# Kernel optimization log

Hardware: AMD Instinct MI355X
Metric: run time of the kernel (lower is better)

The kernel has to match this reference:

```python
import jax, jax.numpy as jnp
import numpy as np

VERY_NEG = -1e11
VERY_SMALL = 1e-10
PAGERANK_LAMBDA = 0.8
FACT_SCALE = 3.0


def _linear(x, W, b):
    return x @ W.T + b


def _lstm(x, Wih, Whh, bih, bhh):
    # single-layer unidirectional LSTM, pytorch gate order (i, f, g, o)
    B, T, _ = x.shape
    H = Whh.shape[1]
    def step(carry, xt):
        h, c = carry
        g = xt @ Wih.T + bih + h @ Whh.T + bhh
        i, f, gg, o = jnp.split(g, 4, axis=-1)
        c = jax.nn.sigmoid(f) * c + jax.nn.sigmoid(i) * jnp.tanh(gg)
        h = jax.nn.sigmoid(o) * jnp.tanh(c)
        return (h, c), h
    init = (jnp.zeros((B, H), x.dtype), jnp.zeros((B, H), x.dtype))
    (h_last, _), hs = jax.lax.scan(step, init, jnp.swapaxes(x, 0, 1))
    return jnp.swapaxes(hs, 0, 1), h_last


def _forward(local_entity, q2e_adj_mat, kb_fact_rel, query_text, e2f_entity, f2e_entity,
             answer_dist, word_emb, entity_emb, rel_emb, ent_W, ent_b, rel_W, rel_b,
             lstm_Wih, lstm_Whh, lstm_bih, lstm_bhh, q2e_W, q2e_b, head_W, head_b,
             tail_W, tail_b, self_W, self_b, e2e_W, e2e_b, score_W, score_b):
    B, E = local_entity.shape
    D = ent_W.shape[0]
    num_word = word_emb.shape[0] - 1
    num_entity = entity_emb.shape[0] - 1
    b_idx = jnp.arange(B)[:, None]  # (B,1) for batched gather/scatter

    # --- query LSTM encoder ---
    query_mask = (query_text != num_word).astype(jnp.float32)            # (B,Q)
    qh, q_last = _lstm(word_emb[query_text], lstm_Wih, lstm_Whh, lstm_bih, lstm_bhh)
    query_node_emb = q_last[:, None, :]                                   # (B,1,D)

    # --- fact embeddings + fact-query attention weights ---
    local_fact_emb = _linear(rel_emb[kb_fact_rel], rel_W, rel_b)          # (B,F,D)
    div = jnp.sqrt(jnp.asarray(D, jnp.float32))
    sim = jnp.einsum('bqd,bfd->bqf', qh, local_fact_emb) / div
    sim = jax.nn.softmax(sim + (1.0 - query_mask)[:, :, None] * VERY_NEG, axis=1)
    att = jnp.einsum('bqf,bqd->bfd', sim, qh)                             # (B,F,D)
    Wf = jnp.sum(att * local_fact_emb, axis=2) / div                      # (B,F)
    W_tilde = jnp.exp(Wf - jnp.max(Wf, axis=1, keepdims=True))
    # e2f_softmax[b,e] = sum of W_tilde over facts whose head is e (sparse e2f^T @ W_tilde)
    e2f_softmax = jnp.maximum(
        jnp.zeros((B, E), jnp.float32).at[b_idx, e2f_entity].add(W_tilde), VERY_SMALL)

    # --- entity embeddings (word_dim != entity_dim -> entity_linear) ---
    local_entity_emb = _linear(entity_emb[local_entity], ent_W, ent_b)    # (B,E,D)
    pagerank_f = q2e_adj_mat[:, :, 0]                                     # (B,E)

    n_layer = q2e_W.shape[0]
    for i in range(n_layer):
        q2e_emb = jnp.broadcast_to(_linear(query_node_emb, q2e_W[i], q2e_b[i]), (B, E, D))
        # entity -> fact: gather head-entity messages
        head = _linear(local_entity_emb, head_W[i], head_b[i])            # (B,E,D)
        e2f_emb = jax.nn.relu(
            _linear(local_fact_emb, self_W[i], self_b[i]) + head[b_idx, e2f_entity])
        pr = pagerank_f / e2f_softmax                                     # (B,E)
        e2f_norm = (W_tilde * pr[b_idx, e2f_entity])[:, :, None]          # (B,F,1)
        e2f_emb = e2f_emb * e2f_norm
        # fact -> entity: scatter-add to tail entities
        tail = _linear(e2f_emb, tail_W[i], tail_b[i])                     # (B,F,D)
        f2e_emb = jax.nn.relu(
            _linear(local_entity_emb, self_W[i], self_b[i])
            + jnp.zeros((B, E, D), jnp.float32).at[b_idx, f2e_entity].add(tail))
        pagerank_f = (PAGERANK_LAMBDA
                      * jnp.zeros((B, E), jnp.float32).at[b_idx, f2e_entity].add(e2f_norm[:, :, 0])
                      + (1.0 - PAGERANK_LAMBDA) * pagerank_f)
        nxt = jnp.concatenate([local_entity_emb, q2e_emb, FACT_SCALE * f2e_emb], axis=2)
        local_entity_emb = jax.nn.relu(_linear(nxt, e2e_W[i], e2e_b[i]))

    score = local_entity_emb @ score_W + score_b                          # (B,E)
    mask = (local_entity != num_entity).astype(jnp.float32)
    score = score + (1.0 - mask) * VERY_NEG
    return jax.nn.sigmoid(score) * mask


def setup_inputs() -> dict:
    key = jax.random.key(0)
    ks = jax.random.split(key, 24)
    B, E, Fc, Q = 8, 2000, 12000, 20
    WD, D = 300, 100
    NE, NW, NR, L = 100000, 40000, 300, 3
    f32 = jnp.float32
    def nrm(k, shape, scale):
        return jax.random.normal(k, shape, f32) * scale
    return {
        'local_entity': jax.random.randint(ks[0], (B, E), 0, NE),
        'q2e_adj_mat': jax.random.uniform(ks[1], (B, E, 1), f32),
        'kb_fact_rel': jax.random.randint(ks[2], (B, Fc), 0, NR),
        'query_text': jax.random.randint(ks[3], (B, Q), 0, NW),
        'e2f_entity': jax.random.randint(ks[4], (B, Fc), 0, E),
        'f2e_entity': jax.random.randint(ks[5], (B, Fc), 0, E),
        'answer_dist': jax.random.uniform(ks[6], (B, E), f32),
        'word_emb': nrm(ks[7], (NW + 1, WD), 0.02),
        'entity_emb': nrm(ks[8], (NE + 1, WD), 0.02),
        'rel_emb': nrm(ks[9], (NR + 1, 2 * WD), 0.02),
        'ent_W': nrm(ks[10], (D, WD), WD ** -0.5), 'ent_b': jnp.zeros((D,), f32),
        'rel_W': nrm(ks[11], (D, 2 * WD), (2 * WD) ** -0.5), 'rel_b': jnp.zeros((D,), f32),
        'lstm_Wih': nrm(ks[12], (4 * D, WD), WD ** -0.5),
        'lstm_Whh': nrm(ks[13], (4 * D, D), D ** -0.5),
        'lstm_bih': jnp.zeros((4 * D,), f32), 'lstm_bhh': jnp.zeros((4 * D,), f32),
        'q2e_W': nrm(ks[14], (L, D, D), D ** -0.5), 'q2e_b': jnp.zeros((L, D), f32),
        'head_W': nrm(ks[15], (L, D, D), D ** -0.5), 'head_b': jnp.zeros((L, D), f32),
        'tail_W': nrm(ks[16], (L, D, D), D ** -0.5), 'tail_b': jnp.zeros((L, D), f32),
        'self_W': nrm(ks[17], (L, D, D), D ** -0.5), 'self_b': jnp.zeros((L, D), f32),
        'e2e_W': nrm(ks[18], (L, D, 3 * D), (3 * D) ** -0.5), 'e2e_b': jnp.zeros((L, D), f32),
        'score_W': nrm(ks[19], (D,), D ** -0.5), 'score_b': jnp.zeros((), f32),
    }


def reference(local_entity, q2e_adj_mat, kb_fact_rel, query_text, e2f_entity, f2e_entity,
              answer_dist, word_emb, entity_emb, rel_emb, ent_W, ent_b, rel_W, rel_b,
              lstm_Wih, lstm_Whh, lstm_bih, lstm_bhh, q2e_W, q2e_b, head_W, head_b,
              tail_W, tail_b, self_W, self_b, e2e_W, e2e_b, score_W, score_b):
    return _forward(local_entity, q2e_adj_mat, kb_fact_rel, query_text, e2f_entity,
                    f2e_entity, answer_dist, word_emb, entity_emb, rel_emb, ent_W, ent_b,
                    rel_W, rel_b, lstm_Wih, lstm_Whh, lstm_bih, lstm_bhh, q2e_W, q2e_b,
                    head_W, head_b, tail_W, tail_b, self_W, self_b, e2e_W, e2e_b,
                    score_W, score_b)
```

## Files before the change

### kernel.cpp

```cpp
#include <hip/hip_runtime.h>
#include <math.h>

#define VERY_NEG  -100000000000.0f
#define VERY_SMALLF 1e-10f

constexpr int B  = 8;
constexpr int E  = 2000;
constexpr int FC = 12000;
constexpr int Q  = 20;
constexpr int WD = 300;
constexpr int D  = 100;
constexpr int NW = 40000;
constexpr int NE = 100000;
constexpr int G4 = 4 * D;
constexpr int NREL = 301;
constexpr int NF = B * FC;
constexpr int NR_ = B * E;
constexpr int NRP = 16384;

__device__ __forceinline__ float sigmoidf_(float x) { return 1.0f / (1.0f + expf(-x)); }

__device__ __forceinline__ void tile16(const float* __restrict__ As_, const float* __restrict__ Bs_,
                                       int rg, int cgc, float acc[4][4]) {
#pragma unroll 5
    for (int k4 = 0; k4 < 25; ++k4) {
        float a_[4][4], b_[4][4];
#pragma unroll
        for (int i = 0; i < 4; ++i) {
            float4 v = *(const float4*)&As_[(rg * 4 + i) * 104 + k4 * 4];
            a_[i][0] = v.x; a_[i][1] = v.y; a_[i][2] = v.z; a_[i][3] = v.w;
        }
#pragma unroll
        for (int kk = 0; kk < 4; ++kk) {
            float4 v = *(const float4*)&Bs_[(k4 * 4 + kk) * 100 + cgc * 4];
            b_[kk][0] = v.x; b_[kk][1] = v.y; b_[kk][2] = v.z; b_[kk][3] = v.w;
        }
#pragma unroll
        for (int kk = 0; kk < 4; ++kk)
#pragma unroll
            for (int i = 0; i < 4; ++i)
#pragma unroll
                for (int j = 0; j < 4; ++j)
                    acc[i][j] += a_[i][kk] * b_[kk][j];
    }
}

__device__ __forceinline__ void tile8(const float* __restrict__ As_, const float* __restrict__ Bs_,
                                      int rg, int cgc, float acc[2][4]) {
#pragma unroll 5
    for (int k4 = 0; k4 < 25; ++k4) {
        float a_[2][4], b_[4][4];
#pragma unroll
        for (int i = 0; i < 2; ++i) {
            float4 v = *(const float4*)&As_[(rg * 2 + i) * 104 + k4 * 4];
            a_[i][0] = v.x; a_[i][1] = v.y; a_[i][2] = v.z; a_[i][3] = v.w;
        }
#pragma unroll
        for (int kk = 0; kk < 4; ++kk) {
            float4 v = *(const float4*)&Bs_[(k4 * 4 + kk) * 100 + cgc * 4];
            b_[kk][0] = v.x; b_[kk][1] = v.y; b_[kk][2] = v.z; b_[kk][3] = v.w;
        }
#pragma unroll
        for (int kk = 0; kk < 4; ++kk)
#pragma unroll
            for (int i = 0; i < 2; ++i)
#pragma unroll
                for (int j = 0; j < 4; ++j)
                    acc[i][j] += a_[i][kk] * b_[kk][j];
    }
}

__device__ __forceinline__ void stage_B100(const float* __restrict__ Wt, int ldW, int col0, int k0,
                                           float* __restrict__ Bs_) {
    for (int i = threadIdx.x; i < 2500; i += 256) {
        int k = i / 25, d2 = i - k * 25;
        *(float4*)&Bs_[k * 100 + d2 * 4] = *(const float4*)&Wt[(size_t)(k0 + k) * ldW + col0 + d2 * 4];
    }
}

__device__ void gemm_tile_g(const float* __restrict__ A, int K,
                            const int* __restrict__ rix, int nrows,
                            const float* __restrict__ Wt, int ldW, int col0,
                            const float* __restrict__ bias,
                            float* __restrict__ C,
                            int base, float* As_, float* Bs_) {
    int tid = threadIdx.x;
    int cg_ = tid & 31, rg = tid >> 5, cgc = cg_ < 25 ? cg_ : 24;
    float acc[4][4] = {{0.f}};
    for (int k0 = 0; k0 < K; k0 += 100) {
        __syncthreads();
        for (int i = tid; i < 800; i += 256) {
            int r = i / 25, c = i - r * 25;
            int rr = base + r; if (rr >= nrows) rr = nrows - 1;
            int gr = rix ? rix[rr] : rr;
            *(float4*)&As_[r * 104 + c * 4] = *(const float4*)&A[(size_t)gr * K + k0 + c * 4];
        }
        stage_B100(Wt, ldW, col0, k0, Bs_);
        __syncthreads();
        tile16(As_, Bs_, rg, cgc, acc);
    }
    if (cg_ < 25) {
        float4 bb = *(const float4*)&bias[col0 + cg_ * 4];
#pragma unroll
        for (int i = 0; i < 4; ++i) {
            int r = base + rg * 4 + i;
            if (r < nrows) {
                float4 o;
                o.x = acc[i][0] + bb.x; o.y = acc[i][1] + bb.y;
                o.z = acc[i][2] + bb.z; o.w = acc[i][3] + bb.w;
                *(float4*)&C[(size_t)r * ldW + col0 + cg_ * 4] = o;
            }
        }
    }
}

__device__ void gemm_tile_512(const float* __restrict__ A, int K,
                              const int* __restrict__ rix, int nrows,
                              const float* __restrict__ Wt, int ldW, int col0,
                              const float* __restrict__ bias,
                              float* __restrict__ C,
                              int base, float* As_, float* Bs_) {
    int tid = threadIdx.x;
    int cg_ = tid & 31, rg = (tid >> 5) & 7, cgc = cg_ < 25 ? cg_ : 24;
    bool on = tid < 256;
    float acc[4][4] = {{0.f}};
    for (int k0 = 0; k0 < K; k0 += 100) {
        __syncthreads();
        for (int i = tid; i < 800; i += 512) {
            int r = i / 25, c = i - r * 25;
            int rr = base + r; if (rr >= nrows) rr = nrows - 1;
            int gr = rix ? rix[rr] : rr;
            *(float4*)&As_[r * 104 + c * 4] = *(const float4*)&A[(size_t)gr * K + k0 + c * 4];
        }
        for (int i = tid; i < 2500; i += 512) {
            int k = i / 25, d2 = i - k * 25;
            *(float4*)&Bs_[k * 100 + d2 * 4] = *(const float4*)&Wt[(size_t)(k0 + k) * ldW + col0 + d2 * 4];
        }
        __syncthreads();
        if (on) tile16(As_, Bs_, rg, cgc, acc);
    }
    if (on && cg_ < 25) {
        float4 bb = *(const float4*)&bias[col0 + cg_ * 4];
#pragma unroll
        for (int i = 0; i < 4; ++i) {
            int r = base + rg * 4 + i;
            if (r < nrows) {
                float4 o;
                o.x = acc[i][0] + bb.x; o.y = acc[i][1] + bb.y;
                o.z = acc[i][2] + bb.z; o.w = acc[i][3] + bb.w;
                *(float4*)&C[(size_t)r * ldW + col0 + cg_ * 4] = o;
            }
        }
    }
}

struct P0 {
    const float *ent_W, *rel_W, *Wih, *Whh, *head_W, *self_W, *tail_W, *e2e_W, *bih, *bhh, *q2e_adj;
    float *entWt, *relWt, *WihT, *WhhT, *headWt, *selfWt, *tailWt, *e2eWt, *bihh, *pr, *e2f_sm;
    const int *f2e, *kb_rel; int *cnt, *present;
};

__device__ void tr_tile(const float* __restrict__ in, float* __restrict__ out, int M, int K,
                        int kx, int my, float tb[32][33]) {
    int x = threadIdx.x & 31, y = threadIdx.x >> 5;
    int k0 = kx * 32, m0 = my * 32;
    for (int yy = y; yy < 32; yy += 8) {
        int m = m0 + yy, k = k0 + x;
        if (m < M && k < K) tb[yy][x] = in[(size_t)m * K + k];
    }
    __syncthreads();
    for (int yy = y; yy < 32; yy += 8) {
        int k = k0 + yy, m = m0 + x;
        if (m < M && k < K) out[(size_t)k * M + m] = tb[x][yy];
    }
}

__global__ __launch_bounds__(256) void k_prep0(P0 p) {
    __shared__ float tb[32][33];
    int j = blockIdx.x, tid = threadIdx.x;
    if (j < 40)       { tr_tile(p.ent_W, p.entWt, 100, 300, j % 10, j / 10, tb); }
    else if (j < 116) { j -= 40;  tr_tile(p.rel_W, p.relWt, 100, 600, j % 19, j / 19, tb); }
    else if (j < 246) { j -= 116; tr_tile(p.Wih, p.WihT, 400, 300, j % 10, j / 10, tb); }
    else if (j < 298) { j -= 246; tr_tile(p.Whh, p.WhhT, 400, 100, j % 4, j / 4, tb); }
    else if (j < 346) { j -= 298; int z = j / 16, t = j % 16; tr_tile(p.head_W + z * 10000, p.headWt + z * 10000, 100, 100, t % 4, t / 4, tb); }
    else if (j < 394) { j -= 346; int z = j / 16, t = j % 16; tr_tile(p.self_W + z * 10000, p.selfWt + z * 10000, 100, 100, t % 4, t / 4, tb); }
    else if (j < 442) { j -= 394; int z = j / 16, t = j % 16; tr_tile(p.tail_W + z * 10000, p.tailWt + z * 10000, 100, 100, t % 4, t / 4, tb); }
    else if (j < 562) { j -= 442; int z = j / 40, t = j % 40; tr_tile(p.e2e_W + z * 30000, p.e2eWt + z * 30000, 100, 300, t % 10, t / 10, tb); }
    else if (j < 564) { int idx = (j - 562) * 256 + tid; if (idx < G4) p.bihh[idx] = p.bih[idx] + p.bhh[idx]; }
    else if (j < 580) { int idx = (j - 564) * 256 + tid; if (idx < 4000) ((float4*)p.pr)[idx] = ((const float4*)p.q2e_adj)[idx]; }
    else if (j < 596) { int idx = (j - 580) * 256 + tid; if (idx < 4000) ((float4*)p.e2f_sm)[idx] = make_float4(0.f, 0.f, 0.f, 0.f); }
    else {
        int fid = (j - 596) * 256 + tid;
        int b = fid / FC;
        atomicAdd(&p.cnt[b * E + p.f2e[fid]], 1);
        p.present[b * NREL + p.kb_rel[fid]] = 1;
    }
}

struct F1P {
    const int *cnt; int *off, *cursor; float *cnt_f;
    const float *word_emb; const int *qtext; const float *WihT, *bihh; float *xW;
    const float *rel_emb, *relWt, *rel_b; float *rel_proj;
    const float *entity_emb; const int *local_entity;
    const float *entWt, *ent_b, *headWt0, *head_b0, *selfWt0, *self_b0;
    float *lee, *head, *lee_self;
};

__device__ void scan_block(const int* __restrict__ cnt, int* __restrict__ off,
                           int* __restrict__ cursor, float* __restrict__ cnt_f, int* part) {
    int t = threadIdx.x;
    int s = 0;
    const int4* c4 = (const int4*)(cnt + t * 64);
#pragma unroll 4
    for (int i = 0; i < 16; ++i) { int4 v = c4[i]; s += v.x + v.y + v.z + v.w; }
    part[t] = s;
    __syncthreads();
    for (int d = 1; d < 256; d <<= 1) {
        int add = (t >= d) ? part[t - d] : 0;
        __syncthreads();
        part[t] += add;
        __syncthreads();
    }
    int run = part[t] - s;
    for (int i = 0; i < 64; ++i) {
        int idx = t * 64 + i;
        if (idx < NR_) {
            off[idx] = run; cursor[idx] = run; cnt_f[idx] = (float)cnt[idx];
            run += cnt[idx];
        }
    }
    if (t == 255) off[NR_] = part[255];
}

__device__ void lee_dual_tile16(int base, const F1P& p, float* As_, float* Bs_) {
    int tid = threadIdx.x;
    int cg_ = tid & 31, rg = tid >> 5, cgc = cg_ < 25 ? cg_ : 24;
    float acc[2][4] = {{0.f}};
    for (int k0 = 0; k0 < 300; k0 += 100) {
        __syncthreads();
        for (int i = tid; i < 400; i += 256) {
            int r = i / 25, c = i - r * 25;
            int gr = p.local_entity[base + r];
            *(float4*)&As_[r * 104 + c * 4] = *(const float4*)&p.entity_emb[(size_t)gr * 300 + k0 + c * 4];
        }
        stage_B100(p.entWt, 100, 0, k0, Bs_);
        __syncthreads();
        tile8(As_, Bs_, rg, cgc, acc);
    }
    __syncthreads();
    if (cg_ < 25) {
        float4 bb = *(const float4*)&p.ent_b[cg_ * 4];
#pragma unroll
        for (int i = 0; i < 2; ++i) {
            int r = base + rg * 2 + i;
            float4 o;
            o.x = acc[i][0] + bb.x; o.y = acc[i][1] + bb.y;
            o.z = acc[i][2] + bb.z; o.w = acc[i][3] + bb.w;
            *(float4*)&p.lee[(size_t)r * 100 + cg_ * 4] = o;
            *(float4*)&As_[(rg * 2 + i) * 104 + cg_ * 4] = o;
        }
    }
    stage_B100(p.headWt0, 100, 0, 0, Bs_);
    __syncthreads();
    float acc2[2][4] = {{0.f}};
    tile8(As_, Bs_, rg, cgc, acc2);
    if (cg_ < 25) {
        float4 bb = *(const float4*)&p.head_b0[cg_ * 4];
#pragma unroll
        for (int i = 0; i < 2; ++i) {
            int r = base + rg * 2 + i;
            float4 o;
            o.x = acc2[i][0] + bb.x; o.y = acc2[i][1] + bb.y;
            o.z = acc2[i][2] + bb.z; o.w = acc2[i][3] + bb.w;
            *(float4*)&p.head[(size_t)r * 100 + cg_ * 4] = o;
        }
    }
    __syncthreads();
    stage_B100(p.selfWt0, 100, 0, 0, Bs_);
    __syncthreads();
    float acc3[2][4] = {{0.f}};
    tile8(As_, Bs_, rg, cgc, acc3);
    if (cg_ < 25) {
        float4 bb = *(const float4*)&p.self_b0[cg_ * 4];
#pragma unroll
        for (int i = 0; i < 2; ++i) {
            int r = base + rg * 2 + i;
            float4 o;
            o.x = acc3[i][0] + bb.x; o.y = acc3[i][1] + bb.y;
            o.z = acc3[i][2] + bb.z; o.w = acc3[i][3] + bb.w;
            *(float4*)&p.lee_self[(size_t)r * 100 + cg_ * 4] = o;
        }
    }
}

__global__ __launch_bounds__(256) void k_front1(F1P p) {
    __shared__ float smem[13328];
    int j = blockIdx.x;
    if (j == 0) {
        scan_block(p.cnt, p.off, p.cursor, p.cnt_f, (int*)smem);
    } else if (j <= 20) {
        j -= 1;
        gemm_tile_g(p.word_emb, WD, p.qtext, B * Q, p.WihT, G4, (j / 5) * 100, p.bihh,
                    p.xW, (j % 5) * 32, smem, smem + 3328);
    } else if (j <= 30) {
        j -= 21;
        gemm_tile_g(p.rel_emb, 2 * WD, nullptr, NREL, p.relWt, D, 0, p.rel_b,
                    p.rel_proj, j * 32, smem, smem + 3328);
    } else {
        lee_dual_tile16((j - 31) * 16, p, smem, smem + 1664);
    }
}

struct F2P {
    const float *xW, *WhhT, *q2e_W, *q2e_b; float *q2e_vec;
    const int *qtext, *present;
    const float *rel_proj; float *Wt_rel;
    const float *selfWt, *self_b; float *self_proj;
};

__device__ void lstm_wfall_block(int b, const F2P& p, float* smem) {
    float* h    = smem;
    float* c    = smem + 128;
    float* gate = smem + 256;
    float* qh_s = smem + 704;
    float* msk  = smem + 2704;
    float* red  = smem + 2752;
    int t = threadIdx.x;
    float w[100];
    if (t < G4) {
#pragma unroll
        for (int j = 0; j < 100; ++j) w[j] = p.WhhT[j * G4 + t];
    }
    if (t < D) { h[t] = 0.f; c[t] = 0.f; }
    if (t < Q) msk[t] = (p.qtext[b * Q + t] != NW) ? 1.f : 0.f;
    __syncthreads();
    for (int step = 0; step < Q; ++step) {
        if (t < G4) {
            float a0 = 0.f, a1 = 0.f, a2 = 0.f, a3 = 0.f;
#pragma unroll
            for (int k4 = 0; k4 < 25; ++k4) {
                float4 hv = *(const float4*)&h[k4 * 4];
                a0 += hv.x * w[k4 * 4 + 0];
                a1 += hv.y * w[k4 * 4 + 1];
                a2 += hv.z * w[k4 * 4 + 2];
                a3 += hv.w * w[k4 * 4 + 3];
            }
            gate[t] = p.xW[(b * Q + step) * G4 + t] + ((a0 + a1) + (a2 + a3));
        }
        __syncthreads();
        if (t < D) {
            float ig = sigmoidf_(gate[t]);
            float fg = sigmoidf_(gate[D + t]);
            float gg = tanhf(gate[2 * D + t]);
            float og = sigmoidf_(gate[3 * D + t]);
            float cn = fg * c[t] + ig * gg;
            c[t] = cn;
            float hn = og * tanhf(cn);
            h[t] = hn;
            qh_s[step * D + t] = hn;
        }
        __syncthreads();
    }
    if (t < 3 * D) {
        int l = t / D, d = t - l * D;
        float acc = p.q2e_b[l * D + d];
        const float* W = p.q2e_W + (size_t)(l * D + d) * D;
        for (int k = 0; k < D; ++k) acc += h[k] * W[k];
        p.q2e_vec[(l * B + b) * D + d] = acc;
    }
    float wf = 0.f;
    bool active = t < NREL;
    if (active) {
        const float* lfe = p.rel_proj + t * D;
        float s[Q];
#pragma unroll
        for (int q = 0; q < Q; ++q) s[q] = 0.f;
        for (int k = 0; k < D; ++k) {
            float lv = lfe[k];
#pragma unroll
            for (int q = 0; q < Q; ++q) s[q] += qh_s[q * D + k] * lv;
        }
        float m = -INFINITY;
        float sv[Q];
#pragma unroll
        for (int q = 0; q < Q; ++q) {
            s[q] *= 0.1f;
            sv[q] = s[q] + (1.f - msk[q]) * VERY_NEG;
            m = fmaxf(m, sv[q]);
        }
        float sum = 0.f;
        float ex[Q];
#pragma unroll
        for (int q = 0; q < Q; ++q) { ex[q] = expf(sv[q] - m); sum += ex[q]; }
#pragma unroll
        for (int q = 0; q < Q; ++q) wf += (ex[q] / sum) * s[q];
    }
    red[t] = (active && p.present[b * NREL + t]) ? wf : -INFINITY;
    __syncthreads();
    for (int st = 256; st > 0; st >>= 1) {
        if (t < st) red[t] = fmaxf(red[t], red[t + st]);
        __syncthreads();
    }
    if (active) p.Wt_rel[b * NREL + t] = expf(wf - red[0]);
}

__global__ __launch_bounds__(512) void k_front2(F2P p) {
    __shared__ float smem[13328];
    int j = blockIdx.x;
    if (j < 8) {
        lstm_wfall_block(j, p, smem);
    } else {
        j -= 8;
        int z = j / 10, t = j % 10;
        gemm_tile_512(p.rel_proj, D, nullptr, NREL, p.selfWt + z * 10000, D, 0, p.self_b + z * 100,
                      p.self_proj + (size_t)z * NREL * D, t * 32, smem, smem + 3328);
    }
}

__global__ void k_scef(const int* __restrict__ f2e, const int* __restrict__ e2f,
                       const int* __restrict__ kb_rel, const float* __restrict__ Wt_rel,
                       int* __restrict__ cursor, int* __restrict__ sorted,
                       float* __restrict__ W_tilde, float* __restrict__ e2f_sm) {
    int fid = blockIdx.x * 256 + threadIdx.x;
    int b = fid / FC;
    int pos = atomicAdd(&cursor[b * E + f2e[fid]], 1);
    sorted[pos] = fid;
    float wt = Wt_rel[b * NREL + kb_rel[fid]];
    W_tilde[fid] = wt;
    atomicAdd(&e2f_sm[b * E + e2f[fid]], wt);
}

__global__ void k_gfact(const int* __restrict__ sorted, const int* __restrict__ kb_rel,
                        const int* __restrict__ e2f, const float* __restrict__ W_tilde,
                        const float* __restrict__ e2f_sm,
                        int* __restrict__ es_rel_s, float* __restrict__ g_s) {
    int j = blockIdx.x * 256 + threadIdx.x;
    if (j >= NF) return;
    int fid = sorted[j];
    int b = fid / FC;
    int es = e2f[fid], rel = kb_rel[fid];
    es_rel_s[j] = es | (rel << 16);
    g_s[j] = W_tilde[fid] / fmaxf(e2f_sm[b * E + es], VERY_SMALLF);
}

__global__ __launch_bounds__(256) void k_gather(const int* __restrict__ es_rel_s,
                                                const float* __restrict__ g_s,
                                                const int* __restrict__ off,
                                                const float* __restrict__ self_proj_l,
                                                const float* __restrict__ head,
                                                const float* __restrict__ pr,
                                                float* __restrict__ u, float* __restrict__ pr_acc) {
    int bid = blockIdx.x;
    int job = (bid & 7) * 500 + (bid >> 3);
    int wave = threadIdx.x >> 6, lane = threadIdx.x & 63;
    int ri = job * 4 + wave;
    int b = ri / E, bE = b * E;
    int s = off[ri], e = off[ri + 1];
    float a0 = 0.f, a1 = 0.f, ns = 0.f;
    const float* hb = head + (size_t)bE * D;
    const float* prb = pr + bE;
    for (int cs = s; cs < e; cs += 64) {
        int cnt = e - cs; if (cnt > 64) cnt = 64;
        int erl = 0; float njl = 0.f;
        if (lane < cnt) {
            erl = es_rel_s[cs + lane];
            njl = g_s[cs + lane] * prb[erl & 0xffff];
        }
        for (int j = 0; j < cnt; ++j) {
            int er = __shfl(erl, j);
            float nj = __shfl(njl, j);
            int es = er & 0xffff, rel = er >> 16;
            const float* sp = self_proj_l + rel * D;
            const float* hr = hb + (size_t)es * D;
            a0 += nj * fmaxf(0.f, sp[lane] + hr[lane]);
            if (lane < 36) a1 += nj * fmaxf(0.f, sp[lane + 64] + hr[lane + 64]);
            ns += nj;
        }
    }
    u[(size_t)ri * D + lane] = a0;
    if (lane < 36) u[(size_t)ri * D + 64 + lane] = a1;
    if (lane == 0) pr_acc[ri] = ns;
}

struct TailP {
    const float *u, *cnt_f, *tailWt_l, *tail_b_l;
    const float *cur, *lee_self_in, *q2e_l, *e2eWt_l, *e2e_b_l;
    const float *pr_acc_c; float *pr; float *nxt;
    const float *headWt_n, *head_b_n, *selfWt_n, *self_b_n;
    float *head, *lee_self_out;
    int last; const int *local_entity; const float *score_W, *score_b; float *out;
};

__global__ __launch_bounds__(256) void k_tailent(TailP p) {
    __shared__ float As_[16 * 104];
    __shared__ float Bs_[100 * 100];
    __shared__ float Fs_[16 * 104];
    int tid = threadIdx.x, base = blockIdx.x * 16;
    int cg_ = tid & 31, rg = tid >> 5, cgc = cg_ < 25 ? cg_ : 24;
    for (int i = tid; i < 400; i += 256) {
        int r = i / 25, c = i - r * 25;
        *(float4*)&As_[r * 104 + c * 4] = *(const float4*)&p.u[(size_t)(base + r) * 100 + c * 4];
    }
    stage_B100(p.tailWt_l, 100, 0, 0, Bs_);
    __syncthreads();
    float accF[2][4] = {{0.f}};
    tile8(As_, Bs_, rg, cgc, accF);
    __syncthreads();
    if (cg_ < 25) {
        float4 tbv = *(const float4*)&p.tail_b_l[cg_ * 4];
#pragma unroll
        for (int i = 0; i < 2; ++i) {
            int r = base + rg * 2 + i;
            float cf = p.cnt_f[r];
            float4 ls = *(const float4*)&p.lee_self_in[(size_t)r * 100 + cg_ * 4];
            float4 o;
            o.x = 3.f * fmaxf(0.f, ls.x + accF[i][0] + cf * tbv.x);
            o.y = 3.f * fmaxf(0.f, ls.y + accF[i][1] + cf * tbv.y);
            o.z = 3.f * fmaxf(0.f, ls.z + accF[i][2] + cf * tbv.z);
            o.w = 3.f * fmaxf(0.f, ls.w + accF[i][3] + cf * tbv.w);
            *(float4*)&Fs_[(rg * 2 + i) * 104 + cg_ * 4] = o;
        }
    }
    if (tid < 16) {
        int r = base + tid;
        p.pr[r] = 0.8f * p.pr_acc_c[r] + 0.2f * p.pr[r];
    }
    float acc[2][4] = {{0.f}};
    __syncthreads();
    for (int i = tid; i < 400; i += 256) {
        int r = i / 25, c = i - r * 25;
        *(float4*)&As_[r * 104 + c * 4] = *(const float4*)&p.cur[(size_t)(base + r) * 100 + c * 4];
    }
    stage_B100(p.e2eWt_l, 100, 0, 0, Bs_);
    __syncthreads();
    tile8(As_, Bs_, rg, cgc, acc);
    __syncthreads();
    for (int i = tid; i < 400; i += 256) {
        int r = i / 25, c = i - r * 25;
        int bb = (base + r) / E;
        *(float4*)&As_[r * 104 + c * 4] = *(const float4*)&p.q2e_l[bb * 100 + c * 4];
    }
    stage_B100(p.e2eWt_l, 100, 0, 100, Bs_);
    __syncthreads();
    tile8(As_, Bs_, rg, cgc, acc);
    __syncthreads();
    stage_B100(p.e2eWt_l, 100, 0, 200, Bs_);
    __syncthreads();
    tile8(Fs_, Bs_, rg, cgc, acc);
    __syncthreads();
    if (cg_ < 25) {
        float4 ebv = *(const float4*)&p.e2e_b_l[cg_ * 4];
#pragma unroll
        for (int i = 0; i < 2; ++i) {
            int r = base + rg * 2 + i;
            float4 o;
            o.x = fmaxf(acc[i][0] + ebv.x, 0.f); o.y = fmaxf(acc[i][1] + ebv.y, 0.f);
            o.z = fmaxf(acc[i][2] + ebv.z, 0.f); o.w = fmaxf(acc[i][3] + ebv.w, 0.f);
            *(float4*)&p.nxt[(size_t)r * 100 + cg_ * 4] = o;
            *(float4*)&As_[(rg * 2 + i) * 104 + cg_ * 4] = o;
        }
    }
    if (!p.last) {
        stage_B100(p.headWt_n, 100, 0, 0, Bs_);
        __syncthreads();
        float a2[2][4] = {{0.f}};
        tile8(As_, Bs_, rg, cgc, a2);
        if (cg_ < 25) {
            float4 bb = *(const float4*)&p.head_b_n[cg_ * 4];
#pragma unroll
            for (int i = 0; i < 2; ++i) {
                int r = base + rg * 2 + i;
                float4 o;
                o.x = a2[i][0] + bb.x; o.y = a2[i][1] + bb.y;
                o.z = a2[i][2] + bb.z; o.w = a2[i][3] + bb.w;
                *(float4*)&p.head[(size_t)r * 100 + cg_ * 4] = o;
            }
        }
        __syncthreads();
        stage_B100(p.selfWt_n, 100, 0, 0, Bs_);
        __syncthreads();
        float a3[2][4] = {{0.f}};
        tile8(As_, Bs_, rg, cgc, a3);
        if (cg_ < 25) {
            float4 bb = *(const float4*)&p.self_b_n[cg_ * 4];
#pragma unroll
            for (int i = 0; i < 2; ++i) {
                int r = base + rg * 2 + i;
                float4 o;
                o.x = a3[i][0] + bb.x; o.y = a3[i][1] + bb.y;
                o.z = a3[i][2] + bb.z; o.w = a3[i][3] + bb.w;
                *(float4*)&p.lee_self_out[(size_t)r * 100 + cg_ * 4] = o;
            }
        }
    } else {
        __syncthreads();
        if (tid < 16) {
            int r = base + tid;
            if (p.local_entity[r] == NE) { p.out[r] = 0.f; }
            else {
                float a = p.score_b[0];
                for (int k = 0; k < D; ++k) a += As_[tid * 104 + k] * p.score_W[k];
                p.out[r] = 1.f / (1.f + expf(-a));
            }
        }
    }
}

extern "C" void kernel_launch(void* const* d_in, const int* in_sizes, int n_in,
                              void* d_out, int out_size, void* d_ws, size_t ws_size,
                              hipStream_t stream) {
    const int*   local_entity = (const int*)d_in[0];
    const float* q2e_adj      = (const float*)d_in[1];
    const int*   kb_rel       = (const int*)d_in[2];
    const int*   qtext        = (const int*)d_in[3];
    const int*   e2f          = (const int*)d_in[4];
    const int*   f2e          = (const int*)d_in[5];
    const float* word_emb     = (const float*)d_in[7];
    const float* entity_emb   = (const float*)d_in[8];
    const float* rel_emb      = (const float*)d_in[9];
    const float* ent_W        = (const float*)d_in[10];
    const float* ent_b        = (const float*)d_in[11];
    const float* rel_W        = (const float*)d_in[12];
    const float* rel_b        = (const float*)d_in[13];
    const float* lstm_Wih     = (const float*)d_in[14];
    const float* lstm_Whh     = (const float*)d_in[15];
    const float* lstm_bih     = (const float*)d_in[16];
    const float* lstm_bhh     = (const float*)d_in[17];
    const float* q2e_W        = (const float*)d_in[18];
    const float* q2e_b        = (const float*)d_in[19];
    const float* head_W       = (const float*)d_in[20];
    const float* head_b       = (const float*)d_in[21];
    const float* tail_W       = (const float*)d_in[22];
    const float* tail_b       = (const float*)d_in[23];
    const float* self_W       = (const float*)d_in[24];
    const float* self_b       = (const float*)d_in[25];
    const float* e2e_W        = (const float*)d_in[26];
    const float* e2e_b        = (const float*)d_in[27];
    const float* score_W      = (const float*)d_in[28];
    const float* score_b      = (const float*)d_in[29];

    float* ws = (float*)d_ws;
    float* rel_proj  = ws;
    float* self_proj = rel_proj  + NREL * D;
    float* xW        = self_proj + 3 * NREL * D;
    float* q2e_vec   = xW        + B * Q * G4;
    float* Wt_rel    = q2e_vec   + 3 * B * D;
    float* W_tilde   = Wt_rel    + B * NREL;
    float* e2f_sm    = W_tilde   + NF;
    float* leeA      = e2f_sm    + NR_;
    float* leeB      = leeA      + NR_ * D;
    float* head      = leeB      + NR_ * D;
    float* lee_self  = head      + NR_ * D;
    float* u_buf     = lee_self  + NR_ * D;
    float* pr        = u_buf     + NR_ * D;
    float* pr_acc    = pr        + NR_;
    float* cnt_f     = pr_acc    + NR_;
    float* g_s       = cnt_f     + NR_;
    float* entWt     = g_s       + NF;
    float* relWt     = entWt     + WD * D;
    float* WihT      = relWt     + 2 * WD * D;
    float* WhhT      = WihT      + WD * G4;
    float* headWt    = WhhT      + D * G4;
    float* selfWt    = headWt    + 3 * D * D;
    float* tailWt    = selfWt    + 3 * D * D;
    float* e2eWt     = tailWt    + 3 * D * D;
    float* bihh      = e2eWt     + 9 * D * D;
    int*   present   = (int*)(bihh + G4);
    int*   cnt       = present   + B * NREL;
    int*   cursor    = cnt       + NRP;
    int*   off       = cursor    + NR_;
    int*   sorted    = off       + NR_ + 1;
    int*   es_rel_s  = sorted    + NF;

    hipMemsetAsync(present, 0, (size_t)(B * NREL + NRP) * sizeof(int), stream);

    P0 p0;
    p0.ent_W = ent_W; p0.rel_W = rel_W; p0.Wih = lstm_Wih; p0.Whh = lstm_Whh;
    p0.head_W = head_W; p0.self_W = self_W; p0.tail_W = tail_W; p0.e2e_W = e2e_W;
    p0.bih = lstm_bih; p0.bhh = lstm_bhh; p0.q2e_adj = q2e_adj;
    p0.entWt = entWt; p0.relWt = relWt; p0.WihT = WihT; p0.WhhT = WhhT;
    p0.headWt = headWt; p0.selfWt = selfWt; p0.tailWt = tailWt; p0.e2eWt = e2eWt;
    p0.bihh = bihh; p0.pr = pr; p0.e2f_sm = e2f_sm;
    p0.f2e = f2e; p0.kb_rel = kb_rel; p0.cnt = cnt; p0.present = present;
    k_prep0<<<971, 256, 0, stream>>>(p0);

    F1P f1;
    f1.cnt = cnt; f1.off = off; f1.cursor = cursor; f1.cnt_f = cnt_f;
    f1.word_emb = word_emb; f1.qtext = qtext; f1.WihT = WihT; f1.bihh = bihh; f1.xW = xW;
    f1.rel_emb = rel_emb; f1.relWt = relWt; f1.rel_b = rel_b; f1.rel_proj = rel_proj;
    f1.entity_emb = entity_emb; f1.local_entity = local_entity;
    f1.entWt = entWt; f1.ent_b = ent_b;
    f1.headWt0 = headWt; f1.head_b0 = head_b; f1.selfWt0 = selfWt; f1.self_b0 = self_b;
    f1.lee = leeA; f1.head = head; f1.lee_self = lee_self;
    k_front1<<<31 + 1000, 256, 0, stream>>>(f1);

    F2P f2;
    f2.xW = xW; f2.WhhT = WhhT; f2.q2e_W = q2e_W; f2.q2e_b = q2e_b; f2.q2e_vec = q2e_vec;
    f2.qtext = qtext; f2.present = present;
    f2.rel_proj = rel_proj; f2.Wt_rel = Wt_rel;
    f2.selfWt = selfWt; f2.self_b = self_b; f2.self_proj = self_proj;
    k_front2<<<38, 512, 0, stream>>>(f2);

    k_scef<<<375, 256, 0, stream>>>(f2e, e2f, kb_rel, Wt_rel, cursor, sorted, W_tilde, e2f_sm);
    k_gfact<<<375, 256, 0, stream>>>(sorted, kb_rel, e2f, W_tilde, e2f_sm, es_rel_s, g_s);

    float* cur = leeA; float* nxt = leeB;
    for (int l = 0; l < 3; ++l) {
        k_gather<<<4000, 256, 0, stream>>>(es_rel_s, g_s, off, self_proj + (size_t)l * NREL * D,
                                           head, pr, u_buf, pr_acc);
        TailP tp;
        tp.u = u_buf; tp.cnt_f = cnt_f;
        tp.tailWt_l = tailWt + l * 10000; tp.tail_b_l = tail_b + l * 100;
        tp.cur = cur; tp.lee_self_in = lee_self; tp.q2e_l = q2e_vec + l * B * D;
        tp.e2eWt_l = e2eWt + l * 30000; tp.e2e_b_l = e2e_b + l * 100;
        tp.pr_acc_c = pr_acc; tp.pr = pr; tp.nxt = nxt;
        int ln = (l < 2) ? l + 1 : l;
        tp.headWt_n = headWt + ln * 10000; tp.head_b_n = head_b + ln * 100;
        tp.selfWt_n = selfWt + ln * 10000; tp.self_b_n = self_b + ln * 100;
        tp.head = head; tp.lee_self_out = lee_self;
        tp.last = (l == 2); tp.local_entity = local_entity;
        tp.score_W = score_W; tp.score_b = score_b; tp.out = (float*)d_out;
        k_tailent<<<1000, 256, 0, stream>>>(tp);
        float* t = cur; cur = nxt; nxt = t;
    }
}
```

Before: 365.4 us.

## Double entity tile to 32 rows with 512-thread blocks in front1 and tailent

The entity-row kernels (k_front1's lee path and k_tailent) now use 512-thread blocks handling 32 rows each instead of 256 threads and 16 rows. The 100x100 weight tile in shared memory is therefore shared by twice as many rows, halving the weight staging traffic and the block count. The query and relation GEMM tiles move to the 512-thread gemm variant, and the scan is guarded so only 256 threads work. The cost is larger per-block shared memory and fewer blocks, which may lower occupancy.

```diff
diff --git a/kernel.cpp b/kernel.cpp
--- a/kernel.cpp
+++ b/kernel.cpp
@@ -70,47 +70,11 @@
     }
 }
 
-__device__ __forceinline__ void stage_B100(const float* __restrict__ Wt, int ldW, int col0, int k0,
-                                           float* __restrict__ Bs_) {
-    for (int i = threadIdx.x; i < 2500; i += 256) {
+__device__ __forceinline__ void stage_B100_512(const float* __restrict__ Wt, int ldW, int col0, int k0,
+                                               float* __restrict__ Bs_) {
+    for (int i = threadIdx.x; i < 2500; i += 512) {
         int k = i / 25, d2 = i - k * 25;
         *(float4*)&Bs_[k * 100 + d2 * 4] = *(const float4*)&Wt[(size_t)(k0 + k) * ldW + col0 + d2 * 4];
-    }
-}
-
-__device__ void gemm_tile_g(const float* __restrict__ A, int K,
-                            const int* __restrict__ rix, int nrows,
-                            const float* __restrict__ Wt, int ldW, int col0,
-                            const float* __restrict__ bias,
-                            float* __restrict__ C,
-                            int base, float* As_, float* Bs_) {
-    int tid = threadIdx.x;
-    int cg_ = tid & 31, rg = tid >> 5, cgc = cg_ < 25 ? cg_ : 24;
-    float acc[4][4] = {{0.f}};
-    for (int k0 = 0; k0 < K; k0 += 100) {
-        __syncthreads();
-        for (int i = tid; i < 800; i += 256) {
-            int r = i / 25, c = i - r * 25;
-            int rr = base + r; if (rr >= nrows) rr = nrows - 1;
-            int gr = rix ? rix[rr] : rr;
-            *(float4*)&As_[r * 104 + c * 4] = *(const float4*)&A[(size_t)gr * K + k0 + c * 4];
-        }
-        stage_B100(Wt, ldW, col0, k0, Bs_);
-        __syncthreads();
-        tile16(As_, Bs_, rg, cgc, acc);
-    }
-    if (cg_ < 25) {
-        float4 bb = *(const float4*)&bias[col0 + cg_ * 4];
-#pragma unroll
-        for (int i = 0; i < 4; ++i) {
-            int r = base + rg * 4 + i;
-            if (r < nrows) {
-                float4 o;
-                o.x = acc[i][0] + bb.x; o.y = acc[i][1] + bb.y;
-                o.z = acc[i][2] + bb.z; o.w = acc[i][3] + bb.w;
-                *(float4*)&C[(size_t)r * ldW + col0 + cg_ * 4] = o;
-            }
-        }
     }
 }
 
@@ -132,10 +96,7 @@
             int gr = rix ? rix[rr] : rr;
             *(float4*)&As_[r * 104 + c * 4] = *(const float4*)&A[(size_t)gr * K + k0 + c * 4];
         }
-        for (int i = tid; i < 2500; i += 512) {
-            int k = i / 25, d2 = i - k * 25;
-            *(float4*)&Bs_[k * 100 + d2 * 4] = *(const float4*)&Wt[(size_t)(k0 + k) * ldW + col0 + d2 * 4];
-        }
+        stage_B100_512(Wt, ldW, col0, k0, Bs_);
         __syncthreads();
         if (on) tile16(As_, Bs_, rg, cgc, acc);
     }
@@ -210,10 +171,12 @@
                            int* __restrict__ cursor, float* __restrict__ cnt_f, int* part) {
     int t = threadIdx.x;
     int s = 0;
-    const int4* c4 = (const int4*)(cnt + t * 64);
+    if (t < 256) {
+        const int4* c4 = (const int4*)(cnt + t * 64);
 #pragma unroll 4
-    for (int i = 0; i < 16; ++i) { int4 v = c4[i]; s += v.x + v.y + v.z + v.w; }
-    part[t] = s;
+        for (int i = 0; i < 16; ++i) { int4 v = c4[i]; s += v.x + v.y + v.z + v.w; }
+    }
+    part[t] = (t < 256) ? s : 0;
     __syncthreads();
     for (int d = 1; d < 256; d <<= 1) {
         int add = (t >= d) ? part[t - d] : 0;
@@ -221,29 +184,32 @@
         part[t] += add;
         __syncthreads();
     }
-    int run = part[t] - s;
-    for (int i = 0; i < 64; ++i) {
-        int idx = t * 64 + i;
-        if (idx < NR_) {
-            off[idx] = run; cursor[idx] = run; cnt_f[idx] = (float)cnt[idx];
-            run += cnt[idx];
+    if (t < 256) {
+        int run = part[t] - s;
+        for (int i = 0; i < 64; ++i) {
+            int idx = t * 64 + i;
+            if (idx < NR_) {
+                off[idx] = run; cursor[idx] = run; cnt_f[idx] = (float)cnt[idx];
+                run += cnt[idx];
+            }
         }
     }
     if (t == 255) off[NR_] = part[255];
 }
 
-__device__ void lee_dual_tile16(int base, const F1P& p, float* As_, float* Bs_) {
+__device__ void lee_dual_tile32(int base, const F1P& p, float* As_, float* Bs_) {
     int tid = threadIdx.x;
-    int cg_ = tid & 31, rg = tid >> 5, cgc = cg_ < 25 ? cg_ : 24;
+    int cg_ = tid & 31, rg = tid >> 5;
+    int cgc = cg_ < 25 ? cg_ : 24;
     float acc[2][4] = {{0.f}};
     for (int k0 = 0; k0 < 300; k0 += 100) {
         __syncthreads();
-        for (int i = tid; i < 400; i += 256) {
+        for (int i = tid; i < 800; i += 512) {
             int r = i / 25, c = i - r * 25;
             int gr = p.local_entity[base + r];
             *(float4*)&As_[r * 104 + c * 4] = *(const float4*)&p.entity_emb[(size_t)gr * 300 + k0 + c * 4];
         }
-        stage_B100(p.entWt, 100, 0, k0, Bs_);
+        stage_B100_512(p.entWt, 100, 0, k0, Bs_);
         __syncthreads();
         tile8(As_, Bs_, rg, cgc, acc);
     }
@@ -260,7 +226,7 @@
             *(float4*)&As_[(rg * 2 + i) * 104 + cg_ * 4] = o;
         }
     }
-    stage_B100(p.headWt0, 100, 0, 0, Bs_);
+    stage_B100_512(p.headWt0, 100, 0, 0, Bs_);
     __syncthreads();
     float acc2[2][4] = {{0.f}};
     tile8(As_, Bs_, rg, cgc, acc2);
@@ -276,7 +242,7 @@
         }
     }
     __syncthreads();
-    stage_B100(p.selfWt0, 100, 0, 0, Bs_);
+    stage_B100_512(p.selfWt0, 100, 0, 0, Bs_);
     __syncthreads();
     float acc3[2][4] = {{0.f}};
     tile8(As_, Bs_, rg, cgc, acc3);
@@ -293,21 +259,21 @@
     }
 }
 
-__global__ __launch_bounds__(256) void k_front1(F1P p) {
+__global__ __launch_bounds__(512) void k_front1(F1P p) {
     __shared__ float smem[13328];
     int j = blockIdx.x;
     if (j == 0) {
         scan_block(p.cnt, p.off, p.cursor, p.cnt_f, (int*)smem);
     } else if (j <= 20) {
         j -= 1;
-        gemm_tile_g(p.word_emb, WD, p.qtext, B * Q, p.WihT, G4, (j / 5) * 100, p.bihh,
-                    p.xW, (j % 5) * 32, smem, smem + 3328);
+        gemm_tile_512(p.word_emb, WD, p.qtext, B * Q, p.WihT, G4, (j / 5) * 100, p.bihh,
+                      p.xW, (j % 5) * 32, smem, smem + 3328);
     } else if (j <= 30) {
         j -= 21;
-        gemm_tile_g(p.rel_emb, 2 * WD, nullptr, NREL, p.relWt, D, 0, p.rel_b,
-                    p.rel_proj, j * 32, smem, smem + 3328);
+        gemm_tile_512(p.rel_emb, 2 * WD, nullptr, NREL, p.relWt, D, 0, p.rel_b,
+                      p.rel_proj, j * 32, smem, smem + 3328);
     } else {
-        lee_dual_tile16((j - 31) * 16, p, smem, smem + 1664);
+        lee_dual_tile32((j - 31) * 32, p, smem, smem + 3328);
     }
 }
 
@@ -491,17 +457,18 @@
     int last; const int *local_entity; const float *score_W, *score_b; float *out;
 };
 
-__global__ __launch_bounds__(256) void k_tailent(TailP p) {
-    __shared__ float As_[16 * 104];
+__global__ __launch_bounds__(512) void k_tailent(TailP p) {
+    __shared__ float As_[32 * 104];
     __shared__ float Bs_[100 * 100];
-    __shared__ float Fs_[16 * 104];
-    int tid = threadIdx.x, base = blockIdx.x * 16;
-    int cg_ = tid & 31, rg = tid >> 5, cgc = cg_ < 25 ? cg_ : 24;
-    for (int i = tid; i < 400; i += 256) {
+    __shared__ float Fs_[32 * 104];
+    int tid = threadIdx.x, base = blockIdx.x * 32;
+    int cg_ = tid & 31, rg = tid >> 5;
+    int cgc = cg_ < 25 ? cg_ : 24;
+    for (int i = tid; i < 800; i += 512) {
         int r = i / 25, c = i - r * 25;
         *(float4*)&As_[r * 104 + c * 4] = *(const float4*)&p.u[(size_t)(base + r) * 100 + c * 4];
     }
-    stage_B100(p.tailWt_l, 100, 0, 0, Bs_);
+    stage_B100_512(p.tailWt_l, 100, 0, 0, Bs_);
     __syncthreads();
     float accF[2][4] = {{0.f}};
     tile8(As_, Bs_, rg, cgc, accF);
@@ -521,30 +488,30 @@
             *(float4*)&Fs_[(rg * 2 + i) * 104 + cg_ * 4] = o;
         }
     }
-    if (tid < 16) {
+    if (tid < 32) {
         int r = base + tid;
         p.pr[r] = 0.8f * p.pr_acc_c[r] + 0.2f * p.pr[r];
     }
     float acc[2][4] = {{0.f}};
     __syncthreads();
-    for (int i = tid; i < 400; i += 256) {
+    for (int i = tid; i < 800; i += 512) {
         int r = i / 25, c = i - r * 25;
         *(float4*)&As_[r * 104 + c * 4] = *(const float4*)&p.cur[(size_t)(base + r) * 100 + c * 4];
     }
-    stage_B100(p.e2eWt_l, 100, 0, 0, Bs_);
+    stage_B100_512(p.e2eWt_l, 100, 0, 0, Bs_);
     __syncthreads();
     tile8(As_, Bs_, rg, cgc, acc);
     __syncthreads();
-    for (int i = tid; i < 400; i += 256) {
+    for (int i = tid; i < 800; i += 512) {
         int r = i / 25, c = i - r * 25;
         int bb = (base + r) / E;
         *(float4*)&As_[r * 104 + c * 4] = *(const float4*)&p.q2e_l[bb * 100 + c * 4];
     }
-    stage_B100(p.e2eWt_l, 100, 0, 100, Bs_);
+    stage_B100_512(p.e2eWt_l, 100, 0, 100, Bs_);
     __syncthreads();
     tile8(As_, Bs_, rg, cgc, acc);
     __syncthreads();
-    stage_B100(p.e2eWt_l, 100, 0, 200, Bs_);
+    stage_B100_512(p.e2eWt_l, 100, 0, 200, Bs_);
     __syncthreads();
     tile8(Fs_, Bs_, rg, cgc, acc);
     __syncthreads();
@@ -561,7 +528,7 @@
         }
     }
     if (!p.last) {
-        stage_B100(p.headWt_n, 100, 0, 0, Bs_);
+        stage_B100_512(p.headWt_n, 100, 0, 0, Bs_);
         __syncthreads();
         float a2[2][4] = {{0.f}};
         tile8(As_, Bs_, rg, cgc, a2);
@@ -577,7 +544,7 @@
             }
         }
         __syncthreads();
-        stage_B100(p.selfWt_n, 100, 0, 0, Bs_);
+        stage_B100_512(p.selfWt_n, 100, 0, 0, Bs_);
         __syncthreads();
         float a3[2][4] = {{0.f}};
         tile8(As_, Bs_, rg, cgc, a3);
@@ -594,7 +561,7 @@
         }
     } else {
         __syncthreads();
-        if (tid < 16) {
+        if (tid < 32) {
             int r = base + tid;
             if (p.local_entity[r] == NE) { p.out[r] = 0.f; }
             else {
@@ -692,7 +659,7 @@
     f1.entWt = entWt; f1.ent_b = ent_b;
     f1.headWt0 = headWt; f1.head_b0 = head_b; f1.selfWt0 = selfWt; f1.self_b0 = self_b;
     f1.lee = leeA; f1.head = head; f1.lee_self = lee_self;
-    k_front1<<<31 + 1000, 256, 0, stream>>>(f1);
+    k_front1<<<531, 512, 0, stream>>>(f1);
 
     F2P f2;
     f2.xW = xW; f2.WhhT = WhhT; f2.q2e_W = q2e_W; f2.q2e_b = q2e_b; f2.q2e_vec = q2e_vec;
@@ -720,7 +687,7 @@
         tp.head = head; tp.lee_self_out = lee_self;
         tp.last = (l == 2); tp.local_entity = local_entity;
         tp.score_W = score_W; tp.score_b = score_b; tp.out = (float*)d_out;
-        k_tailent<<<1000, 256, 0, stream>>>(tp);
+        k_tailent<<<500, 512, 0, stream>>>(tp);
         float* t = cur; cur = nxt; nxt = t;
     }
 }
```

Measured after the change: 299.7 us (median of 2 runs). -18.0%, faster.
